# Optimization experiments

Hardware: AMD Instinct MI355X
Metric: run time of the kernel (lower is better)

Reference implementation:

```python
import jax, jax.numpy as jnp
import numpy as np

B, T, IN, H, OUT = 4096, 512, 4, 64, 1


def setup_inputs() -> dict:
    key = jax.random.key(0)
    ks = jax.random.split(key, 12)
    s_in = 1.0 / np.sqrt(H)
    u = lambda k, shape: jax.random.uniform(k, shape, jnp.float32, -s_in, s_in)
    return {
        "x": jax.random.normal(ks[0], (B, T, IN), jnp.float32),
        "W_ih0": u(ks[1], (4 * H, IN)),
        "W_hh0": u(ks[2], (4 * H, H)),
        "b_ih0": u(ks[3], (4 * H,)),
        "b_hh0": u(ks[4], (4 * H,)),
        "W_ih1": u(ks[5], (4 * H, H)),
        "W_hh1": u(ks[6], (4 * H, H)),
        "b_ih1": u(ks[7], (4 * H,)),
        "b_hh1": u(ks[8], (4 * H,)),
        "W_fc": u(ks[9], (OUT, H)),
        "b_fc": u(ks[10], (OUT,)),
    }


def _lstm_layer(x_seq, W_ih, W_hh, b_ih, b_hh):
    # x_seq: [B, T, D]. PyTorch gate order: i, f, g, o.
    # Precompute input projection for all timesteps (one big GEMM).
    x_proj = jnp.einsum("btd,gd->btg", x_seq, W_ih) + b_ih + b_hh  # [B, T, 4H]
    x_proj = jnp.swapaxes(x_proj, 0, 1)  # [T, B, 4H]
    Bsz = x_seq.shape[0]
    h0 = jnp.zeros((Bsz, W_hh.shape[1]), x_seq.dtype)
    c0 = jnp.zeros_like(h0)

    def step(carry, xp):
        h, c = carry
        gates = xp + h @ W_hh.T  # [B, 4H]
        i, f, g, o = jnp.split(gates, 4, axis=-1)
        i = jax.nn.sigmoid(i)
        f = jax.nn.sigmoid(f)
        g = jnp.tanh(g)
        o = jax.nn.sigmoid(o)
        c_new = f * c + i * g
        h_new = o * jnp.tanh(c_new)
        return (h_new, c_new), h_new

    (hT, cT), h_seq = jax.lax.scan(step, (h0, c0), x_proj)
    return jnp.swapaxes(h_seq, 0, 1), hT  # [B, T, H], [B, H]


def reference(x, W_ih0, W_hh0, b_ih0, b_hh0, W_ih1, W_hh1, b_ih1, b_hh1, W_fc, b_fc):
    h1_seq, _ = _lstm_layer(x, W_ih0, W_hh0, b_ih0, b_hh0)
    _, h2_last = _lstm_layer(h1_seq, W_ih1, W_hh1, b_ih1, b_hh1)
    return h2_last @ W_fc.T + b_fc  # [B, 1]
```

## Files before the change

kernel.cpp:

```cpp
#include <hip/hip_runtime.h>

#define TSEQ 512
#define NTH  512

typedef __attribute__((ext_vector_type(8))) _Float16 half8;
typedef __attribute__((ext_vector_type(4))) float f32x4;
typedef __attribute__((ext_vector_type(4))) unsigned int u32x4;

__device__ __forceinline__ unsigned pkrtz(float a, float b) {
    return __builtin_bit_cast(unsigned, __builtin_amdgcn_cvt_pkrtz(a, b));
}
__device__ __forceinline__ unsigned packF16x2(float a, float b) {
    _Float16 ha = (_Float16)a, hb = (_Float16)b;
    return (unsigned)__builtin_bit_cast(unsigned short, ha) |
           ((unsigned)__builtin_bit_cast(unsigned short, hb) << 16);
}
__device__ __forceinline__ half8 packA16s(const float w8[8], float s) {
    u32x4 W = { packF16x2(w8[0]*s, w8[1]*s), packF16x2(w8[2]*s, w8[3]*s),
                packF16x2(w8[4]*s, w8[5]*s), packF16x2(w8[6]*s, w8[7]*s) };
    return __builtin_bit_cast(half8, W);
}

#define MFMA(a, b, c) __builtin_amdgcn_mfma_f32_16x16x32_f16((a), (b), (c), 0, 0, 0)
#define LD128H(p) __builtin_bit_cast(half8, *(const u32x4*)(p))
#define EXP2(v) __builtin_amdgcn_exp2f(v)
#define RCP(v)  __builtin_amdgcn_rcpf(v)

__global__ __launch_bounds__(NTH, 1)
void lstm2_mfma(const float* __restrict__ x,
                const float* __restrict__ W_ih0, const float* __restrict__ W_hh0,
                const float* __restrict__ b_ih0, const float* __restrict__ b_hh0,
                const float* __restrict__ W_ih1, const float* __restrict__ W_hh1,
                const float* __restrict__ b_ih1, const float* __restrict__ b_hh1,
                const float* __restrict__ W_fc,  const float* __restrict__ b_fc,
                float* __restrict__ out)
{
    const int tid  = threadIdx.x;
    const int lane = tid & 63;
    const int wv   = tid >> 6;
    const int rl   = lane & 15;
    const int g    = lane >> 4;
    const int b0   = blockIdx.x * 16;

    const float NL2E  = -1.44269504088896340736f;
    const float PL2E2 =  2.88539008177792681472f;
    const float L2E2  =  2.88539008177792681472f;

    __shared__ unsigned h0P0[512], h0P1[512];
    __shared__ unsigned h1P0[512], h1P1[512];
    __shared__ float fcl[64 * 17];

    for (int i2 = tid; i2 < 512; i2 += NTH) {
        h0P0[i2] = 0u; h0P1[i2] = 0u; h1P0[i2] = 0u; h1P1[i2] = 0u;
    }
    __syncthreads();

    const int offL = rl*32 + (((g + rl) & 7) << 2);
    const int offH = rl*32 + (((4 + g + rl) & 7) << 2);
    const int q0w  = 8*((wv & 3)) + 2*g;
    const int woff = rl*32 + ((((q0w >> 2) + rl) & 7) << 2) + (q0w & 3);

    if (wv < 4) {
        const int w = wv;
        half8 A0[4][2];
        half8 Ax[4];
        f32x4 bias4[4];
        #pragma unroll
        for (int G = 0; G < 4; ++G) {
            const float sc = (G == 2) ? PL2E2 : NL2E;
            const int row = 64*G + 16*w + rl;
            #pragma unroll
            for (int s = 0; s < 2; ++s) {
                float w8[8];
                const float* src = W_hh0 + row*64 + s*32 + g*8;
                #pragma unroll
                for (int e = 0; e < 8; ++e) w8[e] = src[e];
                A0[G][s] = packA16s(w8, sc);
            }
            {
                u32x4 ax = {0u, 0u, 0u, 0u};
                if (g == 0) {
                    ax.x = packF16x2(W_ih0[row*4+0]*sc, W_ih0[row*4+1]*sc);
                    ax.y = packF16x2(W_ih0[row*4+2]*sc, W_ih0[row*4+3]*sc);
                }
                Ax[G] = __builtin_bit_cast(half8, ax);
            }
            const int rb = 64*G + 16*w + 4*g;
            bias4[G].x = (b_ih0[rb+0] + b_hh0[rb+0]) * sc;
            bias4[G].y = (b_ih0[rb+1] + b_hh0[rb+1]) * sc;
            bias4[G].z = (b_ih0[rb+2] + b_hh0[rb+2]) * sc;
            bias4[G].w = (b_ih0[rb+3] + b_hh0[rb+3]) * sc;
        }
        float cst[4] = {0.f, 0.f, 0.f, 0.f};

        f32x4 xf = *(const f32x4*)(x + ((size_t)(b0 + rl) * TSEQ) * 4);
        unsigned bx0 = pkrtz(xf.x, xf.y);
        unsigned bx1 = pkrtz(xf.z, xf.w);

        auto body0 = [&](const unsigned* rP, unsigned* wP, int i) {
            if (i + 1 < TSEQ)
                xf = *(const f32x4*)(x + ((size_t)(b0 + rl) * TSEQ + (i + 1)) * 4);

            half8 B0 = LD128H(rP + offL);
            half8 B1 = LD128H(rP + offH);
            u32x4 tx = {0u, 0u, 0u, 0u};
            if (g == 0) { tx.x = bx0; tx.y = bx1; }
            half8 Bx = __builtin_bit_cast(half8, tx);

            f32x4 a0, a1, a2, a3;
            a0 = MFMA(Ax[0], Bx, bias4[0]);  a1 = MFMA(Ax[1], Bx, bias4[1]);
            a0 = MFMA(A0[0][0], B0, a0);     a1 = MFMA(A0[1][0], B0, a1);
            a0 = MFMA(A0[0][1], B1, a0);     a1 = MFMA(A0[1][1], B1, a1);
            a2 = MFMA(Ax[2], Bx, bias4[2]);  a3 = MFMA(Ax[3], Bx, bias4[3]);
            float e0[4], e1[4];
            #pragma unroll
            for (int j = 0; j < 4; ++j) { e0[j] = EXP2(a0[j]); e1[j] = EXP2(a1[j]); }
            a2 = MFMA(A0[2][0], B0, a2);     a3 = MFMA(A0[3][0], B0, a3);
            a2 = MFMA(A0[2][1], B1, a2);     a3 = MFMA(A0[3][1], B1, a3);
            float e2[4], e3[4];
            #pragma unroll
            for (int j = 0; j < 4; ++j) { e2[j] = EXP2(a2[j]); e3[j] = EXP2(a3[j]); }

            float hv[4];
            #pragma unroll
            for (int j = 0; j < 4; ++j) {
                float sf = RCP(1.0f + e1[j]);
                float ig = (e2[j] - 1.0f) * RCP((1.0f + e0[j]) * (e2[j] + 1.0f));
                float cn = fmaf(cst[j], sf, ig);
                cst[j] = cn;
                float ec = EXP2(cn * L2E2);
                hv[j] = (ec - 1.0f) * RCP((1.0f + e3[j]) * (ec + 1.0f));
            }

            bx0 = pkrtz(xf.x, xf.y);
            bx1 = pkrtz(xf.z, xf.w);

            *(uint2*)(wP + woff) = make_uint2(pkrtz(hv[0], hv[1]), pkrtz(hv[2], hv[3]));
        };

        for (int ii = 0; ii < 256; ++ii) {
            body0(h0P0, h0P1, 2*ii);     __syncthreads();
            body0(h0P1, h0P0, 2*ii + 1); __syncthreads();
        }
        __syncthreads();
        __syncthreads();
    } else {
        const int w = wv - 4;
        half8 A1[4][4];
        f32x4 bias4[4];
        #pragma unroll
        for (int G = 0; G < 4; ++G) {
            const float sc = (G == 2) ? PL2E2 : NL2E;
            const int row = 64*G + 16*w + rl;
            #pragma unroll
            for (int s = 0; s < 4; ++s) {
                float w8[8];
                const float* src = (s < 2) ? (W_ih1 + row*64 + s*32 + g*8)
                                           : (W_hh1 + row*64 + (s-2)*32 + g*8);
                #pragma unroll
                for (int e = 0; e < 8; ++e) w8[e] = src[e];
                A1[G][s] = packA16s(w8, sc);
            }
            const int rb = 64*G + 16*w + 4*g;
            bias4[G].x = (b_ih1[rb+0] + b_hh1[rb+0]) * sc;
            bias4[G].y = (b_ih1[rb+1] + b_hh1[rb+1]) * sc;
            bias4[G].z = (b_ih1[rb+2] + b_hh1[rb+2]) * sc;
            bias4[G].w = (b_ih1[rb+3] + b_hh1[rb+3]) * sc;
        }
        float cst[4] = {0.f, 0.f, 0.f, 0.f};
        const int u0 = 16*w + 4*g;

        half8 pB0 = {}, pB1 = {};

        auto body1 = [&](const unsigned* r1P, unsigned* wP,
                         const unsigned* n0P, bool wrFC) {
            half8 B2 = LD128H(r1P + offL);
            half8 B3 = LD128H(r1P + offH);

            f32x4 a0, a1, a2, a3;
            a0 = MFMA(A1[0][0], pB0, bias4[0]);  a1 = MFMA(A1[1][0], pB0, bias4[1]);
            a0 = MFMA(A1[0][1], pB1, a0);        a1 = MFMA(A1[1][1], pB1, a1);
            a0 = MFMA(A1[0][2], B2, a0);         a1 = MFMA(A1[1][2], B2, a1);
            a0 = MFMA(A1[0][3], B3, a0);         a1 = MFMA(A1[1][3], B3, a1);
            a2 = MFMA(A1[2][0], pB0, bias4[2]);  a3 = MFMA(A1[3][0], pB0, bias4[3]);
            float e0[4], e1[4];
            #pragma unroll
            for (int j = 0; j < 4; ++j) { e0[j] = EXP2(a0[j]); e1[j] = EXP2(a1[j]); }
            a2 = MFMA(A1[2][1], pB1, a2);        a3 = MFMA(A1[3][1], pB1, a3);
            a2 = MFMA(A1[2][2], B2, a2);         a3 = MFMA(A1[3][2], B2, a3);
            a2 = MFMA(A1[2][3], B3, a2);         a3 = MFMA(A1[3][3], B3, a3);
            float e2[4], e3[4];
            #pragma unroll
            for (int j = 0; j < 4; ++j) { e2[j] = EXP2(a2[j]); e3[j] = EXP2(a3[j]); }

            pB0 = LD128H(n0P + offL);
            pB1 = LD128H(n0P + offH);

            float hv[4];
            #pragma unroll
            for (int j = 0; j < 4; ++j) {
                float sf = RCP(1.0f + e1[j]);
                float ig = (e2[j] - 1.0f) * RCP((1.0f + e0[j]) * (e2[j] + 1.0f));
                float cn = fmaf(cst[j], sf, ig);
                cst[j] = cn;
                float ec = EXP2(cn * L2E2);
                hv[j] = (ec - 1.0f) * RCP((1.0f + e3[j]) * (ec + 1.0f));
            }
            *(uint2*)(wP + woff) = make_uint2(pkrtz(hv[0], hv[1]), pkrtz(hv[2], hv[3]));
            if (wrFC) {
                #pragma unroll
                for (int j = 0; j < 4; ++j) fcl[(u0 + j)*17 + rl] = hv[j];
            }
        };

        __syncthreads();
        pB0 = LD128H(h0P1 + offL);
        pB1 = LD128H(h0P1 + offH);
        __syncthreads();
        for (int ii = 0; ii < 256; ++ii) {
            body1(h1P0, h1P1, h0P0, false);     __syncthreads();
            body1(h1P1, h1P0, h0P1, ii == 255); __syncthreads();
        }
    }

    if (tid < 16) {
        float acc = b_fc[0];
        #pragma unroll 16
        for (int u = 0; u < 64; ++u) acc += fcl[u*17 + tid] * W_fc[u];
        out[b0 + tid] = acc;
    }
}

extern "C" void kernel_launch(void* const* d_in, const int* in_sizes, int n_in,
                              void* d_out, int out_size, void* d_ws, size_t ws_size,
                              hipStream_t stream) {
    const float* x     = (const float*)d_in[0];
    const float* W_ih0 = (const float*)d_in[1];
    const float* W_hh0 = (const float*)d_in[2];
    const float* b_ih0 = (const float*)d_in[3];
    const float* b_hh0 = (const float*)d_in[4];
    const float* W_ih1 = (const float*)d_in[5];
    const float* W_hh1 = (const float*)d_in[6];
    const float* b_ih1 = (const float*)d_in[7];
    const float* b_hh1 = (const float*)d_in[8];
    const float* W_fc  = (const float*)d_in[9];
    const float* b_fc  = (const float*)d_in[10];
    float* out = (float*)d_out;

    dim3 grid(4096 / 16), block(NTH);
    hipLaunchKernelGGL(lstm2_mfma, grid, block, 0, stream,
                       x, W_ih0, W_hh0, b_ih0, b_hh0,
                       W_ih1, W_hh1, b_ih1, b_hh1, W_fc, b_fc, out);
}
```

Measured before the change: 316.8 us.

## Split LSTM gate work across 16 waves with shuffle-based gate exchange

Doubles the block to 1024 threads (8 waves per layer), so each wave computes two 16-row MFMA tiles instead of four. Gate rows are interleaved so that each tile holds two gates, and lanes use a cross-half shuffle to gather all four gates for their hidden units. Each lane then evaluates the activations for two units instead of four. This shortens the serial MFMA chain per timestep, at the cost of shuffles, more barrier participants and extra register pressure under the larger block.

```diff
diff --git a/kernel.cpp b/kernel.cpp
--- a/kernel.cpp
+++ b/kernel.cpp
@@ -1,7 +1,7 @@
 #include <hip/hip_runtime.h>
 
 #define TSEQ 512
-#define NTH  512
+#define NTH  1024
 
 typedef __attribute__((ext_vector_type(8))) _Float16 half8;
 typedef __attribute__((ext_vector_type(4))) float f32x4;
@@ -15,7 +15,7 @@
     return (unsigned)__builtin_bit_cast(unsigned short, ha) |
            ((unsigned)__builtin_bit_cast(unsigned short, hb) << 16);
 }
-__device__ __forceinline__ half8 packA16s(const float w8[8], float s) {
+__device__ __forceinline__ half8 packA16s(const float* w8, float s) {
     u32x4 W = { packF16x2(w8[0]*s, w8[1]*s), packF16x2(w8[2]*s, w8[3]*s),
                 packF16x2(w8[4]*s, w8[5]*s), packF16x2(w8[6]*s, w8[7]*s) };
     return __builtin_bit_cast(half8, W);
@@ -25,6 +25,20 @@
 #define LD128H(p) __builtin_bit_cast(half8, *(const u32x4*)(p))
 #define EXP2(v) __builtin_amdgcn_exp2f(v)
 #define RCP(v)  __builtin_amdgcn_rcpf(v)
+
+__device__ __forceinline__ float act_fused(float ai, float af, float ag, float ao, float* c) {
+    const float L2E2 = 2.88539008177792681472f;
+    float ei = EXP2(ai);
+    float ef = EXP2(af);
+    float eg = EXP2(ag);
+    float eo = EXP2(ao);
+    float sf = RCP(1.0f + ef);
+    float ig = (eg - 1.0f) * RCP((1.0f + ei) * (eg + 1.0f));
+    float cn = fmaf(*c, sf, ig);
+    *c = cn;
+    float ec = EXP2(cn * L2E2);
+    return (ec - 1.0f) * RCP((1.0f + eo) * (ec + 1.0f));
+}
 
 __global__ __launch_bounds__(NTH, 1)
 void lstm2_mfma(const float* __restrict__ x,
@@ -40,11 +54,13 @@
     const int wv   = tid >> 6;
     const int rl   = lane & 15;
     const int g    = lane >> 4;
+    const int gsel = g >> 1;
+    const int gand = g & 1;
     const int b0   = blockIdx.x * 16;
+    const int w    = wv & 7;
 
     const float NL2E  = -1.44269504088896340736f;
     const float PL2E2 =  2.88539008177792681472f;
-    const float L2E2  =  2.88539008177792681472f;
 
     __shared__ unsigned h0P0[512], h0P1[512];
     __shared__ unsigned h1P0[512], h1P1[512];
@@ -57,41 +73,40 @@
 
     const int offL = rl*32 + (((g + rl) & 7) << 2);
     const int offH = rl*32 + (((4 + g + rl) & 7) << 2);
-    const int q0w  = 8*((wv & 3)) + 2*g;
-    const int woff = rl*32 + ((((q0w >> 2) + rl) & 7) << 2) + (q0w & 3);
-
-    if (wv < 4) {
-        const int w = wv;
-        half8 A0[4][2];
-        half8 Ax[4];
-        f32x4 bias4[4];
+    const int q    = 4*w + 2*gand + gsel;
+    const int woff = rl*32 + ((((q >> 2) + rl) & 7) << 2) + (q & 3);
+    const int U0   = 8*w + 4*gand + 2*gsel;
+
+
+    if (wv < 8) {
+        half8 A0[2][2];
+        half8 Ax[2];
+        f32x4 bias4[2];
         #pragma unroll
-        for (int G = 0; G < 4; ++G) {
-            const float sc = (G == 2) ? PL2E2 : NL2E;
-            const int row = 64*G + 16*w + rl;
-            #pragma unroll
-            for (int s = 0; s < 2; ++s) {
-                float w8[8];
-                const float* src = W_hh0 + row*64 + s*32 + g*8;
-                #pragma unroll
-                for (int e = 0; e < 8; ++e) w8[e] = src[e];
-                A0[G][s] = packA16s(w8, sc);
-            }
+        for (int T = 0; T < 2; ++T) {
+            const int gateA = 2*T + (rl >> 3);
+            const float sc  = (gateA == 2) ? PL2E2 : NL2E;
+            const int rowA  = 64*gateA + 8*w + (rl & 7);
+            #pragma unroll
+            for (int s = 0; s < 2; ++s)
+                A0[T][s] = packA16s(W_hh0 + rowA*64 + s*32 + g*8, sc);
             {
                 u32x4 ax = {0u, 0u, 0u, 0u};
                 if (g == 0) {
-                    ax.x = packF16x2(W_ih0[row*4+0]*sc, W_ih0[row*4+1]*sc);
-                    ax.y = packF16x2(W_ih0[row*4+2]*sc, W_ih0[row*4+3]*sc);
+                    ax.x = packF16x2(W_ih0[rowA*4+0]*sc, W_ih0[rowA*4+1]*sc);
+                    ax.y = packF16x2(W_ih0[rowA*4+2]*sc, W_ih0[rowA*4+3]*sc);
                 }
-                Ax[G] = __builtin_bit_cast(half8, ax);
-            }
-            const int rb = 64*G + 16*w + 4*g;
-            bias4[G].x = (b_ih0[rb+0] + b_hh0[rb+0]) * sc;
-            bias4[G].y = (b_ih0[rb+1] + b_hh0[rb+1]) * sc;
-            bias4[G].z = (b_ih0[rb+2] + b_hh0[rb+2]) * sc;
-            bias4[G].w = (b_ih0[rb+3] + b_hh0[rb+3]) * sc;
-        }
-        float cst[4] = {0.f, 0.f, 0.f, 0.f};
+                Ax[T] = __builtin_bit_cast(half8, ax);
+            }
+            const int gateC = 2*T + gsel;
+            const float scb = (gateC == 2) ? PL2E2 : NL2E;
+            const int rowC  = 64*gateC + 8*w + 4*gand;
+            bias4[T].x = (b_ih0[rowC+0] + b_hh0[rowC+0]) * scb;
+            bias4[T].y = (b_ih0[rowC+1] + b_hh0[rowC+1]) * scb;
+            bias4[T].z = (b_ih0[rowC+2] + b_hh0[rowC+2]) * scb;
+            bias4[T].w = (b_ih0[rowC+3] + b_hh0[rowC+3]) * scb;
+        }
+        float cst[2] = {0.f, 0.f};
 
         f32x4 xf = *(const f32x4*)(x + ((size_t)(b0 + rl) * TSEQ) * 4);
         unsigned bx0 = pkrtz(xf.x, xf.y);
@@ -107,35 +122,32 @@
             if (g == 0) { tx.x = bx0; tx.y = bx1; }
             half8 Bx = __builtin_bit_cast(half8, tx);
 
-            f32x4 a0, a1, a2, a3;
-            a0 = MFMA(Ax[0], Bx, bias4[0]);  a1 = MFMA(Ax[1], Bx, bias4[1]);
-            a0 = MFMA(A0[0][0], B0, a0);     a1 = MFMA(A0[1][0], B0, a1);
-            a0 = MFMA(A0[0][1], B1, a0);     a1 = MFMA(A0[1][1], B1, a1);
-            a2 = MFMA(Ax[2], Bx, bias4[2]);  a3 = MFMA(Ax[3], Bx, bias4[3]);
-            float e0[4], e1[4];
-            #pragma unroll
-            for (int j = 0; j < 4; ++j) { e0[j] = EXP2(a0[j]); e1[j] = EXP2(a1[j]); }
-            a2 = MFMA(A0[2][0], B0, a2);     a3 = MFMA(A0[3][0], B0, a3);
-            a2 = MFMA(A0[2][1], B1, a2);     a3 = MFMA(A0[3][1], B1, a3);
-            float e2[4], e3[4];
-            #pragma unroll
-            for (int j = 0; j < 4; ++j) { e2[j] = EXP2(a2[j]); e3[j] = EXP2(a3[j]); }
-
-            float hv[4];
+            f32x4 a0, a1;
+            a0 = MFMA(Ax[0], Bx, bias4[0]);   a1 = MFMA(Ax[1], Bx, bias4[1]);
+            a0 = MFMA(A0[0][0], B0, a0);      a1 = MFMA(A0[1][0], B0, a1);
+            a0 = MFMA(A0[0][1], B1, a0);      a1 = MFMA(A0[1][1], B1, a1);
+
+            float p0[4], p1[4];
             #pragma unroll
             for (int j = 0; j < 4; ++j) {
-                float sf = RCP(1.0f + e1[j]);
-                float ig = (e2[j] - 1.0f) * RCP((1.0f + e0[j]) * (e2[j] + 1.0f));
-                float cn = fmaf(cst[j], sf, ig);
-                cst[j] = cn;
-                float ec = EXP2(cn * L2E2);
-                hv[j] = (ec - 1.0f) * RCP((1.0f + e3[j]) * (ec + 1.0f));
+                p0[j] = __shfl_xor(a0[j], 32);
+                p1[j] = __shfl_xor(a1[j], 32);
+            }
+            float hv[2];
+            #pragma unroll
+            for (int k = 0; k < 2; ++k) {
+                const int j = 2*gsel + k;
+                float G0 = gsel ? p0[j] : a0[j];
+                float G1 = gsel ? a0[j] : p0[j];
+                float G2 = gsel ? p1[j] : a1[j];
+                float G3 = gsel ? a1[j] : p1[j];
+                hv[k] = act_fused(G0, G1, G2, G3, &cst[k]);
             }
 
             bx0 = pkrtz(xf.x, xf.y);
             bx1 = pkrtz(xf.z, xf.w);
 
-            *(uint2*)(wP + woff) = make_uint2(pkrtz(hv[0], hv[1]), pkrtz(hv[2], hv[3]));
+            wP[woff] = pkrtz(hv[0], hv[1]);
         };
 
         for (int ii = 0; ii < 256; ++ii) {
@@ -145,30 +157,28 @@
         __syncthreads();
         __syncthreads();
     } else {
-        const int w = wv - 4;
-        half8 A1[4][4];
-        f32x4 bias4[4];
+        half8 A1[2][4];
+        f32x4 bias4[2];
         #pragma unroll
-        for (int G = 0; G < 4; ++G) {
-            const float sc = (G == 2) ? PL2E2 : NL2E;
-            const int row = 64*G + 16*w + rl;
+        for (int T = 0; T < 2; ++T) {
+            const int gateA = 2*T + (rl >> 3);
+            const float sc  = (gateA == 2) ? PL2E2 : NL2E;
+            const int rowA  = 64*gateA + 8*w + (rl & 7);
             #pragma unroll
             for (int s = 0; s < 4; ++s) {
-                float w8[8];
-                const float* src = (s < 2) ? (W_ih1 + row*64 + s*32 + g*8)
-                                           : (W_hh1 + row*64 + (s-2)*32 + g*8);
-                #pragma unroll
-                for (int e = 0; e < 8; ++e) w8[e] = src[e];
-                A1[G][s] = packA16s(w8, sc);
-            }
-            const int rb = 64*G + 16*w + 4*g;
-            bias4[G].x = (b_ih1[rb+0] + b_hh1[rb+0]) * sc;
-            bias4[G].y = (b_ih1[rb+1] + b_hh1[rb+1]) * sc;
-            bias4[G].z = (b_ih1[rb+2] + b_hh1[rb+2]) * sc;
-            bias4[G].w = (b_ih1[rb+3] + b_hh1[rb+3]) * sc;
-        }
-        float cst[4] = {0.f, 0.f, 0.f, 0.f};
-        const int u0 = 16*w + 4*g;
+                const float* src = (s < 2) ? (W_ih1 + rowA*64 + s*32 + g*8)
+                                           : (W_hh1 + rowA*64 + (s-2)*32 + g*8);
+                A1[T][s] = packA16s(src, sc);
+            }
+            const int gateC = 2*T + gsel;
+            const float scb = (gateC == 2) ? PL2E2 : NL2E;
+            const int rowC  = 64*gateC + 8*w + 4*gand;
+            bias4[T].x = (b_ih1[rowC+0] + b_hh1[rowC+0]) * scb;
+            bias4[T].y = (b_ih1[rowC+1] + b_hh1[rowC+1]) * scb;
+            bias4[T].z = (b_ih1[rowC+2] + b_hh1[rowC+2]) * scb;
+            bias4[T].w = (b_ih1[rowC+3] + b_hh1[rowC+3]) * scb;
+        }
+        float cst[2] = {0.f, 0.f};
 
         half8 pB0 = {}, pB1 = {};
 
@@ -177,39 +187,35 @@
             half8 B2 = LD128H(r1P + offL);
             half8 B3 = LD128H(r1P + offH);
 
-            f32x4 a0, a1, a2, a3;
-            a0 = MFMA(A1[0][0], pB0, bias4[0]);  a1 = MFMA(A1[1][0], pB0, bias4[1]);
-            a0 = MFMA(A1[0][1], pB1, a0);        a1 = MFMA(A1[1][1], pB1, a1);
-            a0 = MFMA(A1[0][2], B2, a0);         a1 = MFMA(A1[1][2], B2, a1);
-            a0 = MFMA(A1[0][3], B3, a0);         a1 = MFMA(A1[1][3], B3, a1);
-            a2 = MFMA(A1[2][0], pB0, bias4[2]);  a3 = MFMA(A1[3][0], pB0, bias4[3]);
-            float e0[4], e1[4];
-            #pragma unroll
-            for (int j = 0; j < 4; ++j) { e0[j] = EXP2(a0[j]); e1[j] = EXP2(a1[j]); }
-            a2 = MFMA(A1[2][1], pB1, a2);        a3 = MFMA(A1[3][1], pB1, a3);
-            a2 = MFMA(A1[2][2], B2, a2);         a3 = MFMA(A1[3][2], B2, a3);
-            a2 = MFMA(A1[2][3], B3, a2);         a3 = MFMA(A1[3][3], B3, a3);
-            float e2[4], e3[4];
-            #pragma unroll
-            for (int j = 0; j < 4; ++j) { e2[j] = EXP2(a2[j]); e3[j] = EXP2(a3[j]); }
+            f32x4 a0, a1;
+            a0 = MFMA(A1[0][0], pB0, bias4[0]);   a1 = MFMA(A1[1][0], pB0, bias4[1]);
+            a0 = MFMA(A1[0][1], pB1, a0);         a1 = MFMA(A1[1][1], pB1, a1);
+            a0 = MFMA(A1[0][2], B2, a0);          a1 = MFMA(A1[1][2], B2, a1);
+            a0 = MFMA(A1[0][3], B3, a0);          a1 = MFMA(A1[1][3], B3, a1);
 
             pB0 = LD128H(n0P + offL);
             pB1 = LD128H(n0P + offH);
 
-            float hv[4];
+            float p0[4], p1[4];
             #pragma unroll
             for (int j = 0; j < 4; ++j) {
-                float sf = RCP(1.0f + e1[j]);
-                float ig = (e2[j] - 1.0f) * RCP((1.0f + e0[j]) * (e2[j] + 1.0f));
-                float cn = fmaf(cst[j], sf, ig);
-                cst[j] = cn;
-                float ec = EXP2(cn * L2E2);
-                hv[j] = (ec - 1.0f) * RCP((1.0f + e3[j]) * (ec + 1.0f));
-            }
-            *(uint2*)(wP + woff) = make_uint2(pkrtz(hv[0], hv[1]), pkrtz(hv[2], hv[3]));
+                p0[j] = __shfl_xor(a0[j], 32);
+                p1[j] = __shfl_xor(a1[j], 32);
+            }
+            float hv[2];
+            #pragma unroll
+            for (int k = 0; k < 2; ++k) {
+                const int j = 2*gsel + k;
+                float G0 = gsel ? p0[j] : a0[j];
+                float G1 = gsel ? a0[j] : p0[j];
+                float G2 = gsel ? p1[j] : a1[j];
+                float G3 = gsel ? a1[j] : p1[j];
+                hv[k] = act_fused(G0, G1, G2, G3, &cst[k]);
+            }
+            wP[woff] = pkrtz(hv[0], hv[1]);
             if (wrFC) {
-                #pragma unroll
-                for (int j = 0; j < 4; ++j) fcl[(u0 + j)*17 + rl] = hv[j];
+                fcl[(U0 + 0)*17 + rl] = hv[0];
+                fcl[(U0 + 1)*17 + rl] = hv[1];
             }
         };
 
```

Result: slower. 677.0 us (+113.7%).
